# Kernel optimization log

Hardware: AMD Instinct MI355X
Metric: run time of the kernel (lower is better)

Reference implementation:

```python
import jax, jax.numpy as jnp
import numpy as np

# Production-scale sparse-voxel constants (Waymo-ish stride-8 grid)
N = 1_000_000   # active voxels across the batch
C = 128         # NUM_BEV_FEATURES
B, Z, Y, X = 8, 4, 468, 468  # batch size and spatial_shape (z, y, x)


def setup_inputs() -> dict:
    key = jax.random.key(0)
    kf, kb, kz, ky, kx = jax.random.split(key, 5)
    features = jax.random.normal(kf, (N, C), dtype=jnp.float32)
    b = jax.random.randint(kb, (N,), 0, B, dtype=jnp.int32)
    z = jax.random.randint(kz, (N,), 0, Z, dtype=jnp.int32)
    y = jax.random.randint(ky, (N,), 0, Y, dtype=jnp.int32)
    x = jax.random.randint(kx, (N,), 0, X, dtype=jnp.int32)
    indices = jnp.stack([b, z, y, x], axis=1)  # [N, 4]
    return {"features": features, "indices": indices}


def reference(features, indices):
    """Height compression: drop z, unique over (b, y, x), scatter-add features.

    Mirrors torch.unique(dim=0, return_inverse=True) + index_add_.
    Returns padded outputs of static size N (unique count is data-dependent;
    padded rows have key -1 and zero features / feature mass only where inv points).
    """
    n = features.shape[0]
    b, y, x = indices[:, 0], indices[:, 2], indices[:, 3]
    # Linearize (b, y, x) into a single int32 key; max key B*Y*X ~ 1.75e6 < 2^31.
    keys = (b * (Y * X) + y * X + x).astype(jnp.int32)
    uniq, inv = jnp.unique(keys, size=n, fill_value=-1, return_inverse=True)
    # index_add_ over unique rows == segment_sum with inverse indices
    features_unique = jax.ops.segment_sum(features, inv, num_segments=n)  # [N, C]
    # Decode unique linear keys back to (b, y, x); padded (-1) rows are garbage-marked.
    bb = uniq // (Y * X)
    rem = uniq % (Y * X)
    yy = rem // X
    xx = rem % X
    indices_unique = jnp.stack([bb, yy, xx], axis=1)  # [N, 3]
    return features_unique, indices_unique
```

## Files before the change

kernel.cpp:

```cpp
#include <hip/hip_runtime.h>

#define N_PTS   1000000
#define C_DIM   128
#define B_DIM   8
#define Y_DIM   468
#define X_DIM   468
#define YX      (Y_DIM * X_DIM)
#define KSPACE  (B_DIM * YX)

#define WG   256
#define EPT  8
#define EPB  (WG * EPT)
#define NBLK ((KSPACE + EPB - 1) / EPB)

#define F_BITS 21
#define F_MASK 0x1FFFFFu
#define SINGLE_FLAG (1ull << 63)

__device__ __forceinline__ unsigned long long shfl_up_u64(unsigned long long v, int delta) {
    unsigned lo = (unsigned)v;
    unsigned hi = (unsigned)(v >> 32);
    lo = __shfl_up(lo, delta, 64);
    hi = __shfl_up(hi, delta, 64);
    return ((unsigned long long)hi << 32) | lo;
}

__global__ void zero_u32(unsigned* __restrict__ p, int n) {
    int i = blockIdx.x * blockDim.x + threadIdx.x;
    if (i < n) p[i] = 0u;
}

__global__ void hist_kernel(const int* __restrict__ idx, unsigned* __restrict__ cnt,
                            unsigned* __restrict__ keys, int n) {
    int i = blockIdx.x * blockDim.x + threadIdx.x;
    if (i >= n) return;
    int4 v = ((const int4*)idx)[i];
    unsigned key = (unsigned)(v.x * YX + v.z * X_DIM + v.w);
    keys[i] = key;
    atomicAdd(&cnt[key], 1u);
}

__global__ void scan1_kernel(const unsigned* __restrict__ cnt,
                             unsigned long long* __restrict__ pairs,
                             unsigned long long* __restrict__ bsums, int K) {
    int base = blockIdx.x * EPB + threadIdx.x * EPT;
    unsigned long long p[EPT];
    unsigned cc[EPT];
    unsigned long long run = 0;
#pragma unroll
    for (int j = 0; j < EPT; ++j) {
        int k = base + j;
        unsigned c = (k < K) ? cnt[k] : 0u;
        cc[j] = c;
        unsigned long long pr = (unsigned long long)c
                              | ((unsigned long long)(c ? 1u : 0u) << F_BITS)
                              | ((unsigned long long)(c >= 2u ? 1u : 0u) << (2 * F_BITS));
        p[j] = run;
        run += pr;
    }
    unsigned long long tot = run;
    int lane = threadIdx.x & 63;
    unsigned long long v = tot;
#pragma unroll
    for (int d = 1; d < 64; d <<= 1) {
        unsigned long long nv = shfl_up_u64(v, d);
        if (lane >= d) v += nv;
    }
    __shared__ unsigned long long wsum[WG / 64];
    int wid = threadIdx.x >> 6;
    if (lane == 63) wsum[wid] = v;
    __syncthreads();
    unsigned long long wexcl = 0;
    for (int w = 0; w < wid; ++w) wexcl += wsum[w];
    unsigned long long texcl = wexcl + v - tot;
#pragma unroll
    for (int j = 0; j < EPT; ++j) {
        int k = base + j;
        if (k < K)
            pairs[k] = (texcl + p[j]) | (cc[j] == 1u ? SINGLE_FLAG : 0ull);
    }
    if (threadIdx.x == WG - 1) bsums[blockIdx.x] = wexcl + v;
}

__global__ void scan2_kernel(unsigned long long* __restrict__ bsums, int nb) {
    int t = threadIdx.x;
    unsigned long long orig = (t < nb) ? bsums[t] : 0ull;
    unsigned long long v = orig;
    int lane = t & 63;
#pragma unroll
    for (int d = 1; d < 64; d <<= 1) {
        unsigned long long nv = shfl_up_u64(v, d);
        if (lane >= d) v += nv;
    }
    __shared__ unsigned long long ws[1024 / 64];
    int wid = t >> 6;
    if (lane == 63) ws[wid] = v;
    __syncthreads();
    unsigned long long wexcl = 0;
    for (int w = 0; w < wid; ++w) wexcl += ws[w];
    if (t < nb) bsums[t] = wexcl + v - orig;
    if (t == 1023) {
        unsigned long long tt = 0;
        for (int w = 0; w < 1024 / 64; ++w) tt += ws[w];
        bsums[nb] = tt;
    }
}

__global__ void uniq_kernel(const unsigned* __restrict__ cnt,
                            const unsigned long long* __restrict__ pairs,
                            const unsigned long long* __restrict__ bsums,
                            uint4* __restrict__ wl, float* __restrict__ outI, int K) {
    int k = blockIdx.x * blockDim.x + threadIdx.x;
    if (k >= K) return;
    unsigned c = cnt[k];
    if (c == 0) return;
    unsigned long long pr = (pairs[k] & ~SINGLE_FLAG) + bsums[k >> 11];
    unsigned rank = (unsigned)((pr >> F_BITS) & F_MASK);
    unsigned bb  = (unsigned)k / YX;
    unsigned rem = (unsigned)k % YX;
    outI[(size_t)rank * 3 + 0] = (float)bb;
    outI[(size_t)rank * 3 + 1] = (float)(rem / X_DIM);
    outI[(size_t)rank * 3 + 2] = (float)(rem % X_DIM);
    if (c >= 2) {
        unsigned start = (unsigned)(pr & F_MASK);
        unsigned mslot = (unsigned)((pr >> (2 * F_BITS)) & F_MASK);
        wl[mslot] = make_uint4(start, start + c, (unsigned)k, rank);
    }
}

__global__ void __launch_bounds__(256)
pointscatter_kernel(const float* __restrict__ feat, const unsigned* __restrict__ keys,
                    const unsigned long long* __restrict__ pairs,
                    const unsigned long long* __restrict__ bsums,
                    unsigned* __restrict__ cnt, unsigned* __restrict__ pids,
                    float* __restrict__ outF, int n) {
    int lane = threadIdx.x & 63;
    int wid  = threadIdx.x >> 6;
    int q    = lane >> 4;
    int sub  = lane & 15;
    long p = (long)blockIdx.x * 16 + wid * 4 + q;
    if (p >= n) return;
    unsigned key = keys[p];
    unsigned long long pr = pairs[key];
    if (pr >> 63) {
        pr += bsums[key >> 11];
        unsigned rank = (unsigned)((pr >> F_BITS) & F_MASK);
        const float4* src = (const float4*)(feat + (size_t)p * C_DIM);
        float4*       dst = (float4*)(outF + (size_t)rank * C_DIM);
        float4 v0 = src[sub];
        float4 v1 = src[sub + 16];
        dst[sub]      = v0;
        dst[sub + 16] = v1;
    } else if (sub == 0) {
        unsigned start = (unsigned)((pr + bsums[key >> 11]) & F_MASK);
        unsigned off = atomicSub(&cnt[key], 1u) - 1u;
        pids[start + off] = (unsigned)p;
    }
}

__global__ void __launch_bounds__(256)
multi_pad_kernel(const float* __restrict__ feat, const unsigned* __restrict__ pointIds,
                 const uint4* __restrict__ wl,
                 const unsigned long long* __restrict__ total,
                 float* __restrict__ outF, float* __restrict__ outI, int n) {
    int lane = threadIdx.x & 63;
    int wid  = threadIdx.x >> 6;
    int half = lane >> 5;
    int sub  = lane & 31;
    unsigned long long tot = *total;
    long nU = (long)((tot >> F_BITS) & F_MASK);
    long m  = (long)((tot >> (2 * F_BITS)) & F_MASK);
    long base   = (long)blockIdx.x * 8 + wid * 2 + half;
    long stride = (long)gridDim.x * 8;
    for (long r = base; r < m; r += stride) {
        uint4 d = wl[r];
        float4 acc = make_float4(0.f, 0.f, 0.f, 0.f);
        unsigned j = d.x, e = d.y;
        for (; j + 1 < e; j += 2) {
            unsigned pid0 = pointIds[j];
            unsigned pid1 = pointIds[j + 1];
            float4 v0 = ((const float4*)(feat + (size_t)pid0 * C_DIM))[sub];
            float4 v1 = ((const float4*)(feat + (size_t)pid1 * C_DIM))[sub];
            acc.x += v0.x + v1.x; acc.y += v0.y + v1.y;
            acc.z += v0.z + v1.z; acc.w += v0.w + v1.w;
        }
        if (j < e) {
            unsigned pid = pointIds[j];
            float4 v = ((const float4*)(feat + (size_t)pid * C_DIM))[sub];
            acc.x += v.x; acc.y += v.y; acc.z += v.z; acc.w += v.w;
        }
        ((float4*)(outF + (size_t)d.w * C_DIM))[sub] = acc;
    }
    for (long r = nU + base; r < n; r += stride) {
        ((float4*)(outF + (size_t)r * C_DIM))[sub] = make_float4(0.f, 0.f, 0.f, 0.f);
        if (sub == 0) {
            outI[(size_t)r * 3 + 0] = -1.0f;
            outI[(size_t)r * 3 + 1] = 467.0f;
            outI[(size_t)r * 3 + 2] = 467.0f;
        }
    }
}

extern "C" void kernel_launch(void* const* d_in, const int* in_sizes, int n_in,
                              void* d_out, int out_size, void* d_ws, size_t ws_size,
                              hipStream_t stream) {
    const float* feat = (const float*)d_in[0];
    const int*   idx  = (const int*)d_in[1];
    const int n = in_sizes[0] / C_DIM;
    const int K = KSPACE;

    char* ws = (char*)d_ws;
    size_t off = 0;
    auto take = [&](size_t bytes) {
        size_t cur = off;
        off = (off + bytes + 255) & ~(size_t)255;
        return cur;
    };
    size_t o_cnt    = take((size_t)K * 4);
    size_t o_keys   = take((size_t)n * 4);
    size_t o_pairs  = take((size_t)K * 8);
    size_t o_bsums  = take((size_t)(NBLK + 1) * 8);
    size_t o_pids   = take((size_t)n * 4);
    size_t o_wl     = take((size_t)(n / 2 + 1) * 16);

    unsigned*           cnt    = (unsigned*)(ws + o_cnt);
    unsigned*           keys   = (unsigned*)(ws + o_keys);
    unsigned long long* pairs  = (unsigned long long*)(ws + o_pairs);
    unsigned long long* bsums  = (unsigned long long*)(ws + o_bsums);
    unsigned*           pids   = (unsigned*)(ws + o_pids);
    uint4*              wl     = (uint4*)(ws + o_wl);

    float* outF = (float*)d_out;
    float* outI = outF + (size_t)n * C_DIM;

    zero_u32<<<(K + 255) / 256, 256, 0, stream>>>(cnt, K);
    hist_kernel<<<(n + 255) / 256, 256, 0, stream>>>(idx, cnt, keys, n);
    scan1_kernel<<<NBLK, WG, 0, stream>>>(cnt, pairs, bsums, K);
    scan2_kernel<<<1, 1024, 0, stream>>>(bsums, NBLK);
    uniq_kernel<<<(K + 255) / 256, 256, 0, stream>>>(cnt, pairs, bsums, wl, outI, K);
    pointscatter_kernel<<<(n + 15) / 16, 256, 0, stream>>>(feat, keys, pairs, bsums,
                                                           cnt, pids, outF, n);
    multi_pad_kernel<<<4096, 256, 0, stream>>>(feat, pids, wl, bsums + NBLK, outF, outI, n);
}
```

Measured before the change: 327.9 us.

## Move padding into point-scatter kernel and use nontemporal vector loads/stores

The zero-padding of unused output rows moves from the multi-point reduction kernel into extra blocks of the point-scatter launch. Padding now runs alongside the singleton copies, leaving the multi kernel to do only reductions. All feature copies, reductions and zero stores switch to nontemporal vector loads and stores, and lane-to-row mappings change to 8 lanes per point in scatter and 16 lanes per row in multi. This aims to cut cache pollution from streaming 512 MB of feature traffic and to overlap the padding stores with scatter work. The cost is more work per lane and more registers.

```diff
diff --git a/kernel.cpp b/kernel.cpp
--- a/kernel.cpp
+++ b/kernel.cpp
@@ -16,6 +16,10 @@
 #define F_BITS 21
 #define F_MASK 0x1FFFFFu
 #define SINGLE_FLAG (1ull << 63)
+
+#define PAD_BLOCKS 2048
+
+typedef float f4 __attribute__((ext_vector_type(4)));
 
 __device__ __forceinline__ unsigned long long shfl_up_u64(unsigned long long v, int delta) {
     unsigned lo = (unsigned)v;
@@ -129,75 +133,101 @@
 }
 
 __global__ void __launch_bounds__(256)
-pointscatter_kernel(const float* __restrict__ feat, const unsigned* __restrict__ keys,
-                    const unsigned long long* __restrict__ pairs,
-                    const unsigned long long* __restrict__ bsums,
-                    unsigned* __restrict__ cnt, unsigned* __restrict__ pids,
-                    float* __restrict__ outF, int n) {
+pointscatter_pad_kernel(const float* __restrict__ feat, const unsigned* __restrict__ keys,
+                        const unsigned long long* __restrict__ pairs,
+                        const unsigned long long* __restrict__ bsums,
+                        unsigned* __restrict__ cnt, unsigned* __restrict__ pids,
+                        float* __restrict__ outF, float* __restrict__ outI,
+                        const unsigned long long* __restrict__ total,
+                        int n, int pointBlocks) {
     int lane = threadIdx.x & 63;
     int wid  = threadIdx.x >> 6;
-    int q    = lane >> 4;
-    int sub  = lane & 15;
-    long p = (long)blockIdx.x * 16 + wid * 4 + q;
-    if (p >= n) return;
-    unsigned key = keys[p];
-    unsigned long long pr = pairs[key];
-    if (pr >> 63) {
-        pr += bsums[key >> 11];
-        unsigned rank = (unsigned)((pr >> F_BITS) & F_MASK);
-        const float4* src = (const float4*)(feat + (size_t)p * C_DIM);
-        float4*       dst = (float4*)(outF + (size_t)rank * C_DIM);
-        float4 v0 = src[sub];
-        float4 v1 = src[sub + 16];
-        dst[sub]      = v0;
-        dst[sub + 16] = v1;
-    } else if (sub == 0) {
-        unsigned start = (unsigned)((pr + bsums[key >> 11]) & F_MASK);
-        unsigned off = atomicSub(&cnt[key], 1u) - 1u;
-        pids[start + off] = (unsigned)p;
+    int e    = lane >> 3;
+    int sub  = lane & 7;
+    if ((int)blockIdx.x < pointBlocks) {
+        long p = (long)blockIdx.x * 32 + wid * 8 + e;
+        if (p >= n) return;
+        unsigned key = keys[p];
+        unsigned long long pr = pairs[key];
+        if (pr >> 63) {
+            pr += bsums[key >> 11];
+            unsigned rank = (unsigned)((pr >> F_BITS) & F_MASK);
+            const f4* src = (const f4*)(feat + (size_t)p * C_DIM);
+            f4*       dst = (f4*)(outF + (size_t)rank * C_DIM);
+            f4 v0 = __builtin_nontemporal_load(src + sub);
+            f4 v1 = __builtin_nontemporal_load(src + sub + 8);
+            f4 v2 = __builtin_nontemporal_load(src + sub + 16);
+            f4 v3 = __builtin_nontemporal_load(src + sub + 24);
+            __builtin_nontemporal_store(v0, dst + sub);
+            __builtin_nontemporal_store(v1, dst + sub + 8);
+            __builtin_nontemporal_store(v2, dst + sub + 16);
+            __builtin_nontemporal_store(v3, dst + sub + 24);
+        } else if (sub == 0) {
+            unsigned start = (unsigned)((pr + bsums[key >> 11]) & F_MASK);
+            unsigned off = atomicSub(&cnt[key], 1u) - 1u;
+            pids[start + off] = (unsigned)p;
+        }
+    } else {
+        unsigned long long tot = *total;
+        long nU = (long)((tot >> F_BITS) & F_MASK);
+        long base   = nU + (long)((int)blockIdx.x - pointBlocks) * 32 + wid * 8 + e;
+        long stride = (long)(gridDim.x - pointBlocks) * 32;
+        f4 z = (f4)(0.f);
+        for (long r = base; r < n; r += stride) {
+            f4* dst = (f4*)(outF + (size_t)r * C_DIM);
+            __builtin_nontemporal_store(z, dst + sub);
+            __builtin_nontemporal_store(z, dst + sub + 8);
+            __builtin_nontemporal_store(z, dst + sub + 16);
+            __builtin_nontemporal_store(z, dst + sub + 24);
+            if (sub == 0) {
+                outI[(size_t)r * 3 + 0] = -1.0f;
+                outI[(size_t)r * 3 + 1] = 467.0f;
+                outI[(size_t)r * 3 + 2] = 467.0f;
+            }
+        }
     }
 }
 
 __global__ void __launch_bounds__(256)
-multi_pad_kernel(const float* __restrict__ feat, const unsigned* __restrict__ pointIds,
-                 const uint4* __restrict__ wl,
-                 const unsigned long long* __restrict__ total,
-                 float* __restrict__ outF, float* __restrict__ outI, int n) {
+multi_kernel(const float* __restrict__ feat, const unsigned* __restrict__ pointIds,
+             const uint4* __restrict__ wl,
+             const unsigned long long* __restrict__ total,
+             float* __restrict__ outF) {
     int lane = threadIdx.x & 63;
     int wid  = threadIdx.x >> 6;
-    int half = lane >> 5;
-    int sub  = lane & 31;
-    unsigned long long tot = *total;
-    long nU = (long)((tot >> F_BITS) & F_MASK);
-    long m  = (long)((tot >> (2 * F_BITS)) & F_MASK);
-    long base   = (long)blockIdx.x * 8 + wid * 2 + half;
-    long stride = (long)gridDim.x * 8;
+    int rq   = lane >> 4;
+    int sub  = lane & 15;
+    long m = (long)(((*total) >> (2 * F_BITS)) & F_MASK);
+    long base   = (long)blockIdx.x * 16 + wid * 4 + rq;
+    long stride = (long)gridDim.x * 16;
     for (long r = base; r < m; r += stride) {
         uint4 d = wl[r];
-        float4 acc = make_float4(0.f, 0.f, 0.f, 0.f);
+        f4 a0 = (f4)(0.f);
+        f4 a1 = (f4)(0.f);
         unsigned j = d.x, e = d.y;
         for (; j + 1 < e; j += 2) {
-            unsigned pid0 = pointIds[j];
-            unsigned pid1 = pointIds[j + 1];
-            float4 v0 = ((const float4*)(feat + (size_t)pid0 * C_DIM))[sub];
-            float4 v1 = ((const float4*)(feat + (size_t)pid1 * C_DIM))[sub];
-            acc.x += v0.x + v1.x; acc.y += v0.y + v1.y;
-            acc.z += v0.z + v1.z; acc.w += v0.w + v1.w;
+            unsigned p0 = pointIds[j];
+            unsigned p1 = pointIds[j + 1];
+            const f4* s0 = (const f4*)(feat + (size_t)p0 * C_DIM);
+            const f4* s1 = (const f4*)(feat + (size_t)p1 * C_DIM);
+            f4 v00 = __builtin_nontemporal_load(s0 + sub);
+            f4 v01 = __builtin_nontemporal_load(s0 + sub + 16);
+            f4 v10 = __builtin_nontemporal_load(s1 + sub);
+            f4 v11 = __builtin_nontemporal_load(s1 + sub + 16);
+            a0 += v00 + v10;
+            a1 += v01 + v11;
         }
         if (j < e) {
-            unsigned pid = pointIds[j];
-            float4 v = ((const float4*)(feat + (size_t)pid * C_DIM))[sub];
-            acc.x += v.x; acc.y += v.y; acc.z += v.z; acc.w += v.w;
-        }
-        ((float4*)(outF + (size_t)d.w * C_DIM))[sub] = acc;
-    }
-    for (long r = nU + base; r < n; r += stride) {
-        ((float4*)(outF + (size_t)r * C_DIM))[sub] = make_float4(0.f, 0.f, 0.f, 0.f);
-        if (sub == 0) {
-            outI[(size_t)r * 3 + 0] = -1.0f;
-            outI[(size_t)r * 3 + 1] = 467.0f;
-            outI[(size_t)r * 3 + 2] = 467.0f;
-        }
+            unsigned p0 = pointIds[j];
+            const f4* s0 = (const f4*)(feat + (size_t)p0 * C_DIM);
+            f4 v00 = __builtin_nontemporal_load(s0 + sub);
+            f4 v01 = __builtin_nontemporal_load(s0 + sub + 16);
+            a0 += v00;
+            a1 += v01;
+        }
+        f4* dst = (f4*)(outF + (size_t)d.w * C_DIM);
+        __builtin_nontemporal_store(a0, dst + sub);
+        __builtin_nontemporal_store(a1, dst + sub + 16);
     }
 }
 
@@ -238,7 +268,10 @@
     scan1_kernel<<<NBLK, WG, 0, stream>>>(cnt, pairs, bsums, K);
     scan2_kernel<<<1, 1024, 0, stream>>>(bsums, NBLK);
     uniq_kernel<<<(K + 255) / 256, 256, 0, stream>>>(cnt, pairs, bsums, wl, outI, K);
-    pointscatter_kernel<<<(n + 15) / 16, 256, 0, stream>>>(feat, keys, pairs, bsums,
-                                                           cnt, pids, outF, n);
-    multi_pad_kernel<<<4096, 256, 0, stream>>>(feat, pids, wl, bsums + NBLK, outF, outI, n);
-}
+    {
+        int pointBlocks = (n + 31) / 32;
+        pointscatter_pad_kernel<<<pointBlocks + PAD_BLOCKS, 256, 0, stream>>>(
+            feat, keys, pairs, bsums, cnt, pids, outF, outI, bsums + NBLK, n, pointBlocks);
+    }
+    multi_kernel<<<4096, 256, 0, stream>>>(feat, pids, wl, bsums + NBLK, outF);
+}
```

After: 279.0 us. -14.9%, faster.
